# Kernel optimization log

Measured on AMD Instinct MI355X. Metric: run time of the kernel, lower is better.

Reference implementation:

```python
import jax, jax.numpy as jnp
import numpy as np
import math

SCALE = 16
R_MAX = 4
ALPHA_DYN = 2.0


def _bilinear_down(x, Ho, Wo):
    # torch F.interpolate bilinear, align_corners=False, no antialias. x: [C,H,W]
    C, H, W = x.shape
    def coords(no, ni):
        src = jnp.maximum((jnp.arange(no, dtype=jnp.float32) + 0.5) * (ni / no) - 0.5, 0.0)
        i0 = jnp.floor(src).astype(jnp.int32)
        t = src - i0.astype(jnp.float32)
        return jnp.clip(i0, 0, ni - 1), jnp.clip(i0 + 1, 0, ni - 1), t
    r0, r1, tr = coords(Ho, H)
    c0, c1, tc = coords(Wo, W)
    x = x[:, r0, :] * (1.0 - tr)[None, :, None] + x[:, r1, :] * tr[None, :, None]
    x = x[:, :, c0] * (1.0 - tc)[None, None, :] + x[:, :, c1] * tc[None, None, :]
    return x


def _jbu(feat_lr, guide_hr, sx_raw, sy_raw, th_raw, sr_raw):
    B, C, Hl, Wl = feat_lr.shape
    Hh, Wh = guide_hr.shape[2], guide_hr.shape[3]

    # parameter transforms
    up = lambda p: jnp.repeat(jnp.repeat(p[0, 0], SCALE, axis=0), SCALE, axis=1)  # nearest, exact multiple
    sx = jnp.maximum(up(jnp.exp(sx_raw)), 1e-6)
    sy = jnp.maximum(up(jnp.exp(sy_raw)), 1e-6)
    th = up(math.pi * jnp.tanh(th_raw))
    sr = jnp.maximum(up(jnp.exp(sr_raw)), 1e-6)

    Yh, Xh = jnp.meshgrid(jnp.arange(Hh, dtype=jnp.float32), jnp.arange(Wh, dtype=jnp.float32), indexing='ij')
    uc = jnp.round((Yh + 0.5) / SCALE - 0.5).astype(jnp.int32)
    vc = jnp.round((Xh + 0.5) / SCALE - 0.5).astype(jnp.int32)

    R_map_sq = jnp.clip(ALPHA_DYN * jnp.maximum(sx, sy), 1.0, float(R_MAX)) ** 2
    guide_lr = _bilinear_down(guide_hr[0], Hl, Wl)  # [Cg,Hl,Wl]
    cos_t, sin_t = jnp.cos(th), jnp.sin(th)
    inv2sx2 = 1.0 / (2.0 * sx ** 2 + 1e-8)
    inv2sy2 = 1.0 / (2.0 * sy ** 2 + 1e-8)
    inv2sr2 = 1.0 / (2.0 * sr ** 2 + 1e-8)

    d = jnp.arange(-R_MAX, R_MAX + 1, dtype=jnp.int32)
    dys, dxs = jnp.meshgrid(d, d, indexing='ij')
    offs = jnp.stack([dys.ravel(), dxs.ravel()], axis=1)  # [(2R+1)^2, 2]

    g_hr = guide_hr[0]    # [Cg,Hh,Wh]
    f_lr = feat_lr[0]     # [C,Hl,Wl]

    def step(carry, off):
        num, den = carry
        dy, dx = off[0], off[1]
        ui = jnp.clip(uc + dy, 0, Hl - 1)  # [Hh,Wh] int32
        vi = jnp.clip(vc + dx, 0, Wl - 1)
        cur_dx = (Xh - (vi.astype(jnp.float32) * SCALE + (SCALE - 1) / 2.0)) / SCALE
        cur_dy = (Yh - (ui.astype(jnp.float32) * SCALE + (SCALE - 1) / 2.0)) / SCALE
        a = cur_dx * cos_t + cur_dy * sin_t
        b = -cur_dx * sin_t + cur_dy * cos_t
        g_lr_s = guide_lr[:, ui, vi]                       # [Cg,Hh,Wh] gather
        g_diff2 = jnp.sum((g_hr - g_lr_s) ** 2, axis=0)    # [Hh,Wh]
        log_w = -(a ** 2) * inv2sx2 - (b ** 2) * inv2sy2 - g_diff2 * inv2sr2
        mask = (dy * dy + dx * dx).astype(jnp.float32) <= R_map_sq
        w = jnp.exp(log_w) * mask.astype(jnp.float32)      # [Hh,Wh]
        f_s = f_lr[:, ui, vi]                              # [C,Hh,Wh] gather
        return (num + f_s * w[None], den + w), None

    num0 = jnp.zeros((C, Hh, Wh), jnp.float32)
    den0 = jnp.zeros((Hh, Wh), jnp.float32)
    (num, den), _ = jax.lax.scan(step, (num0, den0), offs)
    res = num / jnp.maximum(den, 1e-8)
    return res[None].astype(feat_lr.dtype)


def setup_inputs() -> dict:
    key = jax.random.key(0)
    k1, k2 = jax.random.split(key)
    feat_lr = jax.random.normal(k1, (1, 128, 32, 32), jnp.float32)
    guide_hr = jax.random.normal(k2, (1, 3, 512, 512), jnp.float32)
    sx_raw = jnp.full((1, 1, 32, 32), float(np.log(16.0)), jnp.float32)
    sy_raw = jnp.full((1, 1, 32, 32), float(np.log(16.0)), jnp.float32)
    th_raw = jnp.zeros((1, 1, 32, 32), jnp.float32)
    sr_raw = jnp.full((1, 1, 32, 32), float(np.log(0.12)), jnp.float32)
    return {"feat_lr": feat_lr, "guide_hr": guide_hr, "sx_raw": sx_raw,
            "sy_raw": sy_raw, "th_raw": th_raw, "sr_raw": sr_raw}


def reference(feat_lr, guide_hr, sx_raw, sy_raw, th_raw, sr_raw):
    return _jbu(feat_lr, guide_hr, sx_raw, sy_raw, th_raw, sr_raw)
```

## Files before the change

### kernel.cpp

```cpp
#include <hip/hip_runtime.h>
#include <math.h>

#define HH 512
#define WH 512
#define L2E 1.44269504f
#define PI_F 3.14159265358979323846f
#define FTK 72

typedef __attribute__((ext_vector_type(8))) short short8v;
typedef __attribute__((ext_vector_type(4))) float float4v;

__device__ const unsigned char ORD[64] = {
    0x44,
    0x34,0x43,0x45,0x54,
    0x33,0x35,0x53,0x55,
    0x24,0x42,0x46,0x64,
    0x23,0x25,0x32,0x36,0x52,0x56,0x63,0x65,
    0x22,0x26,0x62,0x66,
    0x14,0x41,0x47,0x74,
    0x13,0x15,0x31,0x37,0x51,0x57,0x73,0x75,
    0x12,0x16,0x21,0x27,0x61,0x67,0x72,0x76,
    0x04,0x40,0x48,0x84,
    0x03,0x05,0x30,0x38,0x50,0x58,0x83,0x85,
    0x11,0x17,0x71,0x77,
    0x02,0x06,0x20
};

__global__ __launch_bounds__(256) void prep_kernel(
    const float* __restrict__ feat,
    const float* __restrict__ guide,
    float* __restrict__ ws)
{
    const int gid = blockIdx.x * 256 + threadIdx.x;
    float* glr = ws;
    unsigned short* featT = (unsigned short*)(ws + 4096);
    if (gid < 131072) {
        const int cell = gid >> 7;
        const int c    = gid & 127;
        const float v  = feat[c * 1024 + cell];
        const unsigned int b = __float_as_uint(v);
        featT[gid] = (unsigned short)((b + 0x7FFFu + ((b >> 16) & 1u)) >> 16);
    }
    if (gid < 1024) {
        const int u = gid >> 5, v = gid & 31;
        const int y0 = u * 16 + 7, x0 = v * 16 + 7;
        #pragma unroll
        for (int ch = 0; ch < 3; ++ch) {
            const float* g = guide + ch * (HH * WH);
            const float s = g[y0 * WH + x0] + g[y0 * WH + x0 + 1]
                          + g[(y0 + 1) * WH + x0] + g[(y0 + 1) * WH + x0 + 1];
            glr[gid * 4 + ch] = 0.25f * s;
        }
        glr[gid * 4 + 3] = 0.0f;
    }
}

__global__ __launch_bounds__(256, 4) void jbu_kernel(
    const float* __restrict__ guide,
    const float* __restrict__ sx_raw,
    const float* __restrict__ sy_raw,
    const float* __restrict__ th_raw,
    const float* __restrict__ sr_raw,
    const float* __restrict__ ws,
    float* __restrict__ out)
{
    __shared__ __align__(16) unsigned short FT[128 * FTK];
    __shared__ float tabK[64], tabA[64], tabB[64];
    __shared__ float tabG0[64], tabG1[64], tabG2[64];
    __shared__ float hdr[6];

    const float* glr = ws;
    const unsigned short* featT = (const unsigned short*)(ws + 4096);

    const int tid = threadIdx.x;
    const int cell = (blockIdx.x & 7) * 128 + (blockIdx.x >> 3);
    const int cu = cell >> 5, cv = cell & 31;

    if (tid < 64) {
        const int k = tid;
        const float sx  = fmaxf(__expf(sx_raw[cell]), 1e-6f);
        const float sy  = fmaxf(__expf(sy_raw[cell]), 1e-6f);
        const float thv = PI_F * tanhf(th_raw[cell]);
        const float sr  = fmaxf(__expf(sr_raw[cell]), 1e-6f);
        const float R   = fminf(fmaxf(2.0f * fmaxf(sx, sy), 1.0f), 4.0f);
        const float Rsq = R * R;
        const float cth = cosf(thv), sth = sinf(thv);
        const float i2sx = 1.0f / (2.0f * sx * sx + 1e-8f);
        const float i2sy = 1.0f / (2.0f * sy * sy + 1e-8f);
        const float i2sr = 1.0f / (2.0f * sr * sr + 1e-8f);
        if (k == 0) {
            hdr[0] = cth; hdr[1] = sth;
            hdr[2] = i2sx * L2E; hdr[3] = i2sy * L2E; hdr[4] = i2sr * L2E;
            hdr[5] = Rsq;
        }
        const int o  = ORD[k];
        const int dy = (o >> 4) - 4, dx = (o & 15) - 4;
        const int act = ((float)(dy * dy + dx * dx) <= Rsq);
        const int ui = min(max(cu + dy, 0), 31);
        const int vi = min(max(cv + dx, 0), 31);
        const float gl0 = glr[(ui * 32 + vi) * 4 + 0];
        const float gl1 = glr[(ui * 32 + vi) * 4 + 1];
        const float gl2 = glr[(ui * 32 + vi) * 4 + 2];
        const float rk = (float)(vi - cv), tk = (float)(ui - cu);
        const float ak = rk * cth + tk * sth;
        const float bk = tk * cth - rk * sth;
        tabK[k]  = act ? -(ak * ak * i2sx + bk * bk * i2sy
                           + (gl0*gl0 + gl1*gl1 + gl2*gl2) * i2sr) * L2E
                       : -1e30f;
        tabA[k]  = 2.0f * ak * i2sx * L2E;
        tabB[k]  = 2.0f * bk * i2sy * L2E;
        tabG0[k] = 2.0f * gl0 * i2sr * L2E;
        tabG1[k] = 2.0f * gl1 * i2sr * L2E;
        tabG2[k] = 2.0f * gl2 * i2sr * L2E;
    }

    const int wave = tid >> 6;
    const int lane = tid & 63;
    const int lg   = lane >> 4;
    const int pxx  = lane & 15;
    const int mtb  = wave * 4;

    float g0[4], g1[4], g2[4];
    #pragma unroll
    for (int mt = 0; mt < 4; ++mt) {
        const int y = cu * 16 + mtb + mt;
        const int o = y * WH + cv * 16 + pxx;
        g0[mt] = guide[o];
        g1[mt] = guide[HH * WH + o];
        g2[mt] = guide[2 * HH * WH + o];
    }

    #pragma unroll
    for (int it = 0; it < 4; ++it) {
        const int item = it * 256 + tid;
        const int k  = item & 63;
        const int cg = item >> 6;
        const int o  = ORD[k];
        const int ui = min(max(cu + (o >> 4) - 4, 0), 31);
        const int vi = min(max(cv + (o & 15) - 4, 0), 31);
        const uint4 val = *(const uint4*)(featT + (ui * 32 + vi) * 128 + cg * 8);
        const unsigned short* vs = (const unsigned short*)&val;
        #pragma unroll
        for (int j = 0; j < 8; ++j)
            FT[(cg * 8 + j) * FTK + k] = vs[j];
    }
    __syncthreads();

    const float cth = hdr[0], sth = hdr[1];
    const float i2sxl = hdr[2], i2syl = hdr[3], i2srl = hdr[4];
    const bool  use2 = hdr[5] >= 10.0f;
    const float qd = ((float)pxx - 7.5f) * 0.0625f;

    float a0[4], b0[4], P[4];
    #pragma unroll
    for (int mt = 0; mt < 4; ++mt) {
        const float pd = ((float)(mtb + mt) - 7.5f) * 0.0625f;
        a0[mt] = qd * cth + pd * sth;
        b0[mt] = pd * cth - qd * sth;
        P[mt]  = -(a0[mt]*a0[mt]*i2sxl + b0[mt]*b0[mt]*i2syl
                   + (g0[mt]*g0[mt] + g1[mt]*g1[mt] + g2[mt]*g2[mt]) * i2srl);
    }

    short8v Afrag[4][2];
    float den[4] = {0.f, 0.f, 0.f, 0.f};
    #pragma unroll
    for (int ks = 0; ks < 2; ++ks) {
        if (ks == 0 || use2) {
            float cK[8], cA[8], cB[8], cG0[8], cG1[8], cG2[8];
            #pragma unroll
            for (int i = 0; i < 8; ++i) {
                const int k = ks * 32 + lg * 8 + i;
                cK[i] = tabK[k];  cA[i] = tabA[k];  cB[i] = tabB[k];
                cG0[i] = tabG0[k]; cG1[i] = tabG1[k]; cG2[i] = tabG2[k];
            }
            #pragma unroll
            for (int mt = 0; mt < 4; ++mt) {
                short8v av;
                #pragma unroll
                for (int i = 0; i < 8; ++i) {
                    float lw = P[mt] + cK[i];
                    lw = fmaf(a0[mt], cA[i], lw);
                    lw = fmaf(b0[mt], cB[i], lw);
                    lw = fmaf(g0[mt], cG0[i], lw);
                    lw = fmaf(g1[mt], cG1[i], lw);
                    lw = fmaf(g2[mt], cG2[i], lw);
                    const float w = __builtin_amdgcn_exp2f(lw);
                    den[mt] += w;
                    const unsigned int b = __float_as_uint(w);
                    av[i] = (short)((b + 0x7FFFu + ((b >> 16) & 1u)) >> 16);
                }
                Afrag[mt][ks] = av;
            }
        }
    }

    float invd[4][4];
    #pragma unroll
    for (int mt = 0; mt < 4; ++mt) {
        float d = den[mt];
        d += __shfl_xor(d, 16);
        d += __shfl_xor(d, 32);
        const float id = 1.0f / fmaxf(d, 1e-8f);
        #pragma unroll
        for (int r = 0; r < 4; ++r)
            invd[mt][r] = __shfl(id, lg * 4 + r);
    }

    #pragma unroll
    for (int nt = 0; nt < 8; ++nt) {
        const int ch = nt * 16 + pxx;
        short8v Bf0 = *(const short8v*)&FT[ch * FTK + lg * 8];
        short8v Bf1 = *(const short8v*)&FT[ch * FTK + 32 + lg * 8];
        #pragma unroll
        for (int mt = 0; mt < 4; ++mt) {
            float4v acc = {0.f, 0.f, 0.f, 0.f};
            acc = __builtin_amdgcn_mfma_f32_16x16x32_bf16(Afrag[mt][0], Bf0, acc, 0, 0, 0);
            if (use2)
                acc = __builtin_amdgcn_mfma_f32_16x16x32_bf16(Afrag[mt][1], Bf1, acc, 0, 0, 0);
            const int y = cu * 16 + mtb + mt;
            float4v res;
            res[0] = acc[0] * invd[mt][0];
            res[1] = acc[1] * invd[mt][1];
            res[2] = acc[2] * invd[mt][2];
            res[3] = acc[3] * invd[mt][3];
            *(float4v*)(out + (size_t)ch * (HH * WH) + y * WH + cv * 16 + lg * 4) = res;
        }
    }
}

extern "C" void kernel_launch(void* const* d_in, const int* in_sizes, int n_in,
                              void* d_out, int out_size, void* d_ws, size_t ws_size,
                              hipStream_t stream) {
    const float* feat   = (const float*)d_in[0];
    const float* guide  = (const float*)d_in[1];
    const float* sx_raw = (const float*)d_in[2];
    const float* sy_raw = (const float*)d_in[3];
    const float* th_raw = (const float*)d_in[4];
    const float* sr_raw = (const float*)d_in[5];
    float* out = (float*)d_out;
    float* ws  = (float*)d_ws;

    prep_kernel<<<512, 256, 0, stream>>>(feat, guide, ws);
    jbu_kernel<<<1024, 256, 0, stream>>>(guide, sx_raw, sy_raw, th_raw, sr_raw, ws, out);
}
```

Before: 37.64 us.

## Split channels across two blocks per cell and hoist feature loads early

Each output cell is now handled by two blocks, each covering 64 of the 128 channels. This halves the shared feature tile, doubles the grid to 2048 blocks and raises the launch-bounds occupancy hint to 5. Feature gathers and guide loads are issued before the parameter-table setup so their latency overlaps it, and tanh/sincos use fast intrinsics. The cost is that the weight computation (exp2 per pixel and neighbour) is duplicated across the two blocks of each cell.

```diff
diff --git a/kernel.cpp b/kernel.cpp
--- a/kernel.cpp
+++ b/kernel.cpp
@@ -55,7 +55,7 @@
     }
 }
 
-__global__ __launch_bounds__(256, 4) void jbu_kernel(
+__global__ __launch_bounds__(256, 5) void jbu_kernel(
     const float* __restrict__ guide,
     const float* __restrict__ sx_raw,
     const float* __restrict__ sy_raw,
@@ -64,7 +64,7 @@
     const float* __restrict__ ws,
     float* __restrict__ out)
 {
-    __shared__ __align__(16) unsigned short FT[128 * FTK];
+    __shared__ __align__(16) unsigned short FT[64 * FTK];
     __shared__ float tabK[64], tabA[64], tabB[64];
     __shared__ float tabG0[64], tabG1[64], tabG2[64];
     __shared__ float hdr[6];
@@ -73,18 +73,53 @@
     const unsigned short* featT = (const unsigned short*)(ws + 4096);
 
     const int tid = threadIdx.x;
-    const int cell = (blockIdx.x & 7) * 128 + (blockIdx.x >> 3);
+    const int b   = blockIdx.x;
+    const int q    = (b >> 3) & 1;
+    const int cell = (b & 7) * 128 + (b >> 4);
     const int cu = cell >> 5, cv = cell & 31;
+
+    uint4 stg[2];
+    int stgk[2], stgcg[2];
+    #pragma unroll
+    for (int it = 0; it < 2; ++it) {
+        const int item = it * 256 + tid;
+        const int k  = item & 63;
+        const int cg = item >> 6;
+        const int o  = ORD[k];
+        const int ui = min(max(cu + (o >> 4) - 4, 0), 31);
+        const int vi = min(max(cv + (o & 15) - 4, 0), 31);
+        stg[it] = *(const uint4*)(featT + (ui * 32 + vi) * 128 + q * 64 + cg * 8);
+        stgk[it] = k; stgcg[it] = cg;
+    }
+
+    const int wave = tid >> 6;
+    const int lane = tid & 63;
+    const int lg   = lane >> 4;
+    const int pxx  = lane & 15;
+    const int mtb  = wave * 4;
+
+    float g0[4], g1[4], g2[4];
+    #pragma unroll
+    for (int mt = 0; mt < 4; ++mt) {
+        const int y = cu * 16 + mtb + mt;
+        const int o = y * WH + cv * 16 + pxx;
+        g0[mt] = guide[o];
+        g1[mt] = guide[HH * WH + o];
+        g2[mt] = guide[2 * HH * WH + o];
+    }
 
     if (tid < 64) {
         const int k = tid;
         const float sx  = fmaxf(__expf(sx_raw[cell]), 1e-6f);
         const float sy  = fmaxf(__expf(sy_raw[cell]), 1e-6f);
-        const float thv = PI_F * tanhf(th_raw[cell]);
+        const float tr  = fminf(fmaxf(th_raw[cell], -10.f), 10.f);
+        const float e2t = __expf(2.0f * tr);
+        const float thv = PI_F * ((e2t - 1.0f) / (e2t + 1.0f));
         const float sr  = fmaxf(__expf(sr_raw[cell]), 1e-6f);
         const float R   = fminf(fmaxf(2.0f * fmaxf(sx, sy), 1.0f), 4.0f);
         const float Rsq = R * R;
-        const float cth = cosf(thv), sth = sinf(thv);
+        float sth, cth;
+        __sincosf(thv, &sth, &cth);
         const float i2sx = 1.0f / (2.0f * sx * sx + 1e-8f);
         const float i2sy = 1.0f / (2.0f * sy * sy + 1e-8f);
         const float i2sr = 1.0f / (2.0f * sr * sr + 1e-8f);
@@ -114,35 +149,12 @@
         tabG2[k] = 2.0f * gl2 * i2sr * L2E;
     }
 
-    const int wave = tid >> 6;
-    const int lane = tid & 63;
-    const int lg   = lane >> 4;
-    const int pxx  = lane & 15;
-    const int mtb  = wave * 4;
-
-    float g0[4], g1[4], g2[4];
-    #pragma unroll
-    for (int mt = 0; mt < 4; ++mt) {
-        const int y = cu * 16 + mtb + mt;
-        const int o = y * WH + cv * 16 + pxx;
-        g0[mt] = guide[o];
-        g1[mt] = guide[HH * WH + o];
-        g2[mt] = guide[2 * HH * WH + o];
-    }
-
-    #pragma unroll
-    for (int it = 0; it < 4; ++it) {
-        const int item = it * 256 + tid;
-        const int k  = item & 63;
-        const int cg = item >> 6;
-        const int o  = ORD[k];
-        const int ui = min(max(cu + (o >> 4) - 4, 0), 31);
-        const int vi = min(max(cv + (o & 15) - 4, 0), 31);
-        const uint4 val = *(const uint4*)(featT + (ui * 32 + vi) * 128 + cg * 8);
-        const unsigned short* vs = (const unsigned short*)&val;
+    #pragma unroll
+    for (int it = 0; it < 2; ++it) {
+        const unsigned short* vs = (const unsigned short*)&stg[it];
         #pragma unroll
         for (int j = 0; j < 8; ++j)
-            FT[(cg * 8 + j) * FTK + k] = vs[j];
+            FT[(stgcg[it] * 8 + j) * FTK + stgk[it]] = vs[j];
     }
     __syncthreads();
 
@@ -186,8 +198,8 @@
                     lw = fmaf(g2[mt], cG2[i], lw);
                     const float w = __builtin_amdgcn_exp2f(lw);
                     den[mt] += w;
-                    const unsigned int b = __float_as_uint(w);
-                    av[i] = (short)((b + 0x7FFFu + ((b >> 16) & 1u)) >> 16);
+                    const unsigned int bb = __float_as_uint(w);
+                    av[i] = (short)((bb + 0x7FFFu + ((bb >> 16) & 1u)) >> 16);
                 }
                 Afrag[mt][ks] = av;
             }
@@ -207,10 +219,11 @@
     }
 
     #pragma unroll
-    for (int nt = 0; nt < 8; ++nt) {
-        const int ch = nt * 16 + pxx;
-        short8v Bf0 = *(const short8v*)&FT[ch * FTK + lg * 8];
-        short8v Bf1 = *(const short8v*)&FT[ch * FTK + 32 + lg * 8];
+    for (int nt = 0; nt < 4; ++nt) {
+        const int chl = nt * 16 + pxx;
+        short8v Bf0 = *(const short8v*)&FT[chl * FTK + lg * 8];
+        short8v Bf1 = *(const short8v*)&FT[chl * FTK + 32 + lg * 8];
+        const size_t chp = (size_t)(q * 64 + chl) * (HH * WH);
         #pragma unroll
         for (int mt = 0; mt < 4; ++mt) {
             float4v acc = {0.f, 0.f, 0.f, 0.f};
@@ -223,7 +236,7 @@
             res[1] = acc[1] * invd[mt][1];
             res[2] = acc[2] * invd[mt][2];
             res[3] = acc[3] * invd[mt][3];
-            *(float4v*)(out + (size_t)ch * (HH * WH) + y * WH + cv * 16 + lg * 4) = res;
+            *(float4v*)(out + chp + y * WH + cv * 16 + lg * 4) = res;
         }
     }
 }
@@ -241,5 +254,5 @@
     float* ws  = (float*)d_ws;
 
     prep_kernel<<<512, 256, 0, stream>>>(feat, guide, ws);
-    jbu_kernel<<<1024, 256, 0, stream>>>(guide, sx_raw, sy_raw, th_raw, sr_raw, ws, out);
+    jbu_kernel<<<2048, 256, 0, stream>>>(guide, sx_raw, sy_raw, th_raw, sr_raw, ws, out);
 }
```

Result: slower. 56.96 us (+51.3%).

## Process two cells per block and stage outputs in LDS for wider stores

Applied to the files above, without the earlier changes.

Each block now handles two horizontally adjacent low-res cells with 512 threads, and MFMA results are staged through a shared-memory tile so each output row segment is written as 128 contiguous bytes instead of 64-byte pieces. This targets write coalescing of the large 128-channel output. In exchange it adds two block barriers per channel tile and more LDS per block, and the second K-step MFMA now runs whenever either cell needs it. It also swaps tanhf/cosf/sinf for exp-based tanh and __sincosf in the per-cell setup.

```diff
diff --git a/kernel.cpp b/kernel.cpp
--- a/kernel.cpp
+++ b/kernel.cpp
@@ -55,7 +55,7 @@
     }
 }
 
-__global__ __launch_bounds__(256, 4) void jbu_kernel(
+__global__ __launch_bounds__(512, 4) void jbu_kernel(
     const float* __restrict__ guide,
     const float* __restrict__ sx_raw,
     const float* __restrict__ sy_raw,
@@ -64,37 +64,46 @@
     const float* __restrict__ ws,
     float* __restrict__ out)
 {
-    __shared__ __align__(16) unsigned short FT[128 * FTK];
-    __shared__ float tabK[64], tabA[64], tabB[64];
-    __shared__ float tabG0[64], tabG1[64], tabG2[64];
-    __shared__ float hdr[6];
+    __shared__ __align__(16) unsigned short FT[2][128][FTK];
+    __shared__ float tabK[2][64], tabA[2][64], tabB[2][64];
+    __shared__ float tabG0[2][64], tabG1[2][64], tabG2[2][64];
+    __shared__ float hdr[2][8];
+    __shared__ __align__(16) float OutT[16][16][34];
 
     const float* glr = ws;
     const unsigned short* featT = (const unsigned short*)(ws + 4096);
 
     const int tid = threadIdx.x;
-    const int cell = (blockIdx.x & 7) * 128 + (blockIdx.x >> 3);
-    const int cu = cell >> 5, cv = cell & 31;
-
-    if (tid < 64) {
-        const int k = tid;
+    const int b   = blockIdx.x;
+    const int pair = (b & 7) * 64 + (b >> 3);
+    const int cu  = pair >> 4;
+    const int cv0 = (pair & 15) * 2;
+
+    if (tid < 128) {
+        const int c2 = tid >> 6;
+        const int k  = tid & 63;
+        const int cell = cu * 32 + cv0 + c2;
         const float sx  = fmaxf(__expf(sx_raw[cell]), 1e-6f);
         const float sy  = fmaxf(__expf(sy_raw[cell]), 1e-6f);
-        const float thv = PI_F * tanhf(th_raw[cell]);
+        const float tr  = fminf(fmaxf(th_raw[cell], -10.f), 10.f);
+        const float e2t = __expf(2.0f * tr);
+        const float thv = PI_F * ((e2t - 1.0f) / (e2t + 1.0f));
         const float sr  = fmaxf(__expf(sr_raw[cell]), 1e-6f);
         const float R   = fminf(fmaxf(2.0f * fmaxf(sx, sy), 1.0f), 4.0f);
         const float Rsq = R * R;
-        const float cth = cosf(thv), sth = sinf(thv);
+        float sth, cth;
+        __sincosf(thv, &sth, &cth);
         const float i2sx = 1.0f / (2.0f * sx * sx + 1e-8f);
         const float i2sy = 1.0f / (2.0f * sy * sy + 1e-8f);
         const float i2sr = 1.0f / (2.0f * sr * sr + 1e-8f);
         if (k == 0) {
-            hdr[0] = cth; hdr[1] = sth;
-            hdr[2] = i2sx * L2E; hdr[3] = i2sy * L2E; hdr[4] = i2sr * L2E;
-            hdr[5] = Rsq;
+            hdr[c2][0] = cth; hdr[c2][1] = sth;
+            hdr[c2][2] = i2sx * L2E; hdr[c2][3] = i2sy * L2E; hdr[c2][4] = i2sr * L2E;
+            hdr[c2][5] = Rsq;
         }
         const int o  = ORD[k];
         const int dy = (o >> 4) - 4, dx = (o & 15) - 4;
+        const int cv = cv0 + c2;
         const int act = ((float)(dy * dy + dx * dx) <= Rsq);
         const int ui = min(max(cu + dy, 0), 31);
         const int vi = min(max(cv + dx, 0), 31);
@@ -104,21 +113,23 @@
         const float rk = (float)(vi - cv), tk = (float)(ui - cu);
         const float ak = rk * cth + tk * sth;
         const float bk = tk * cth - rk * sth;
-        tabK[k]  = act ? -(ak * ak * i2sx + bk * bk * i2sy
-                           + (gl0*gl0 + gl1*gl1 + gl2*gl2) * i2sr) * L2E
-                       : -1e30f;
-        tabA[k]  = 2.0f * ak * i2sx * L2E;
-        tabB[k]  = 2.0f * bk * i2sy * L2E;
-        tabG0[k] = 2.0f * gl0 * i2sr * L2E;
-        tabG1[k] = 2.0f * gl1 * i2sr * L2E;
-        tabG2[k] = 2.0f * gl2 * i2sr * L2E;
+        tabK[c2][k]  = act ? -(ak * ak * i2sx + bk * bk * i2sy
+                               + (gl0*gl0 + gl1*gl1 + gl2*gl2) * i2sr) * L2E
+                           : -1e30f;
+        tabA[c2][k]  = 2.0f * ak * i2sx * L2E;
+        tabB[c2][k]  = 2.0f * bk * i2sy * L2E;
+        tabG0[c2][k] = 2.0f * gl0 * i2sr * L2E;
+        tabG1[c2][k] = 2.0f * gl1 * i2sr * L2E;
+        tabG2[c2][k] = 2.0f * gl2 * i2sr * L2E;
     }
 
     const int wave = tid >> 6;
     const int lane = tid & 63;
     const int lg   = lane >> 4;
     const int pxx  = lane & 15;
-    const int mtb  = wave * 4;
+    const int c2   = wave >> 2;
+    const int mtb  = (wave & 3) * 4;
+    const int cv   = cv0 + c2;
 
     float g0[4], g1[4], g2[4];
     #pragma unroll
@@ -132,23 +143,24 @@
 
     #pragma unroll
     for (int it = 0; it < 4; ++it) {
-        const int item = it * 256 + tid;
-        const int k  = item & 63;
-        const int cg = item >> 6;
+        const int item = it * 512 + tid;
+        const int k   = item & 63;
+        const int cg  = (item >> 6) & 15;
+        const int c2s = item >> 10;
         const int o  = ORD[k];
         const int ui = min(max(cu + (o >> 4) - 4, 0), 31);
-        const int vi = min(max(cv + (o & 15) - 4, 0), 31);
+        const int vi = min(max(cv0 + c2s + (o & 15) - 4, 0), 31);
         const uint4 val = *(const uint4*)(featT + (ui * 32 + vi) * 128 + cg * 8);
         const unsigned short* vs = (const unsigned short*)&val;
         #pragma unroll
         for (int j = 0; j < 8; ++j)
-            FT[(cg * 8 + j) * FTK + k] = vs[j];
+            FT[c2s][cg * 8 + j][k] = vs[j];
     }
     __syncthreads();
 
-    const float cth = hdr[0], sth = hdr[1];
-    const float i2sxl = hdr[2], i2syl = hdr[3], i2srl = hdr[4];
-    const bool  use2 = hdr[5] >= 10.0f;
+    const float cth = hdr[c2][0], sth = hdr[c2][1];
+    const float i2sxl = hdr[c2][2], i2syl = hdr[c2][3], i2srl = hdr[c2][4];
+    const bool  use2 = (hdr[0][5] >= 10.0f) || (hdr[1][5] >= 10.0f);
     const float qd = ((float)pxx - 7.5f) * 0.0625f;
 
     float a0[4], b0[4], P[4];
@@ -170,8 +182,8 @@
             #pragma unroll
             for (int i = 0; i < 8; ++i) {
                 const int k = ks * 32 + lg * 8 + i;
-                cK[i] = tabK[k];  cA[i] = tabA[k];  cB[i] = tabB[k];
-                cG0[i] = tabG0[k]; cG1[i] = tabG1[k]; cG2[i] = tabG2[k];
+                cK[i] = tabK[c2][k];  cA[i] = tabA[c2][k];  cB[i] = tabB[c2][k];
+                cG0[i] = tabG0[c2][k]; cG1[i] = tabG1[c2][k]; cG2[i] = tabG2[c2][k];
             }
             #pragma unroll
             for (int mt = 0; mt < 4; ++mt) {
@@ -186,8 +198,8 @@
                     lw = fmaf(g2[mt], cG2[i], lw);
                     const float w = __builtin_amdgcn_exp2f(lw);
                     den[mt] += w;
-                    const unsigned int b = __float_as_uint(w);
-                    av[i] = (short)((b + 0x7FFFu + ((b >> 16) & 1u)) >> 16);
+                    const unsigned int bb = __float_as_uint(w);
+                    av[i] = (short)((bb + 0x7FFFu + ((bb >> 16) & 1u)) >> 16);
                 }
                 Afrag[mt][ks] = av;
             }
@@ -206,25 +218,37 @@
             invd[mt][r] = __shfl(id, lg * 4 + r);
     }
 
+    const int pxq   = tid & 7;
+    const int pr    = tid >> 3;
+    const int chs   = pr & 15;
+    const int rowq  = pr >> 4;
     #pragma unroll
     for (int nt = 0; nt < 8; ++nt) {
         const int ch = nt * 16 + pxx;
-        short8v Bf0 = *(const short8v*)&FT[ch * FTK + lg * 8];
-        short8v Bf1 = *(const short8v*)&FT[ch * FTK + 32 + lg * 8];
+        short8v Bf0 = *(const short8v*)&FT[c2][ch][lg * 8];
+        short8v Bf1 = *(const short8v*)&FT[c2][ch][32 + lg * 8];
         #pragma unroll
         for (int mt = 0; mt < 4; ++mt) {
             float4v acc = {0.f, 0.f, 0.f, 0.f};
             acc = __builtin_amdgcn_mfma_f32_16x16x32_bf16(Afrag[mt][0], Bf0, acc, 0, 0, 0);
             if (use2)
                 acc = __builtin_amdgcn_mfma_f32_16x16x32_bf16(Afrag[mt][1], Bf1, acc, 0, 0, 0);
-            const int y = cu * 16 + mtb + mt;
             float4v res;
             res[0] = acc[0] * invd[mt][0];
             res[1] = acc[1] * invd[mt][1];
             res[2] = acc[2] * invd[mt][2];
             res[3] = acc[3] * invd[mt][3];
-            *(float4v*)(out + (size_t)ch * (HH * WH) + y * WH + cv * 16 + lg * 4) = res;
-        }
+            *(float4v*)&OutT[mtb + mt][pxx][c2 * 16 + lg * 4] = res;
+        }
+        __syncthreads();
+        #pragma unroll
+        for (int i = 0; i < 4; ++i) {
+            const int row = i * 4 + rowq;
+            const float4v v = *(const float4v*)&OutT[row][chs][pxq * 4];
+            *(float4v*)(out + (size_t)(nt * 16 + chs) * (HH * WH)
+                        + (cu * 16 + row) * WH + cv0 * 16 + pxq * 4) = v;
+        }
+        __syncthreads();
     }
 }
 
@@ -241,5 +265,5 @@
     float* ws  = (float*)d_ws;
 
     prep_kernel<<<512, 256, 0, stream>>>(feat, guide, ws);
-    jbu_kernel<<<1024, 256, 0, stream>>>(guide, sx_raw, sy_raw, th_raw, sr_raw, ws, out);
+    jbu_kernel<<<512, 512, 0, stream>>>(guide, sx_raw, sy_raw, th_raw, sr_raw, ws, out);
 }
```

New measurement: 42.49 us. 1.13x slower.

## Fuse prep kernel into JBU kernel, computing bf16 features and low-res guide inline

Applied to the files above, without the earlier changes.

Removes the separate prep kernel launch. The main kernel now reads fp32 features directly with a strided gather, converts them to bf16 in-kernel, and computes the 2x2-average low-res guide values on the fly inside the table setup. Each block redoes this conversion for its 64 neighbours, so the redundant reads are uncoalesced (1024-element channel stride), but one launch and a global workspace round trip go away. Transcendentals are also switched to fast intrinsics (__sincosf, exp-based tanh).

```diff
diff --git a/kernel.cpp b/kernel.cpp
--- a/kernel.cpp
+++ b/kernel.cpp
@@ -26,42 +26,13 @@
     0x02,0x06,0x20
 };
 
-__global__ __launch_bounds__(256) void prep_kernel(
+__global__ __launch_bounds__(256, 4) void jbu_fused_kernel(
     const float* __restrict__ feat,
-    const float* __restrict__ guide,
-    float* __restrict__ ws)
-{
-    const int gid = blockIdx.x * 256 + threadIdx.x;
-    float* glr = ws;
-    unsigned short* featT = (unsigned short*)(ws + 4096);
-    if (gid < 131072) {
-        const int cell = gid >> 7;
-        const int c    = gid & 127;
-        const float v  = feat[c * 1024 + cell];
-        const unsigned int b = __float_as_uint(v);
-        featT[gid] = (unsigned short)((b + 0x7FFFu + ((b >> 16) & 1u)) >> 16);
-    }
-    if (gid < 1024) {
-        const int u = gid >> 5, v = gid & 31;
-        const int y0 = u * 16 + 7, x0 = v * 16 + 7;
-        #pragma unroll
-        for (int ch = 0; ch < 3; ++ch) {
-            const float* g = guide + ch * (HH * WH);
-            const float s = g[y0 * WH + x0] + g[y0 * WH + x0 + 1]
-                          + g[(y0 + 1) * WH + x0] + g[(y0 + 1) * WH + x0 + 1];
-            glr[gid * 4 + ch] = 0.25f * s;
-        }
-        glr[gid * 4 + 3] = 0.0f;
-    }
-}
-
-__global__ __launch_bounds__(256, 4) void jbu_kernel(
     const float* __restrict__ guide,
     const float* __restrict__ sx_raw,
     const float* __restrict__ sy_raw,
     const float* __restrict__ th_raw,
     const float* __restrict__ sr_raw,
-    const float* __restrict__ ws,
     float* __restrict__ out)
 {
     __shared__ __align__(16) unsigned short FT[128 * FTK];
@@ -69,22 +40,23 @@
     __shared__ float tabG0[64], tabG1[64], tabG2[64];
     __shared__ float hdr[6];
 
-    const float* glr = ws;
-    const unsigned short* featT = (const unsigned short*)(ws + 4096);
-
     const int tid = threadIdx.x;
-    const int cell = (blockIdx.x & 7) * 128 + (blockIdx.x >> 3);
+    const int b   = blockIdx.x;
+    const int cell = (b & 7) * 128 + (b >> 3);
     const int cu = cell >> 5, cv = cell & 31;
 
     if (tid < 64) {
         const int k = tid;
         const float sx  = fmaxf(__expf(sx_raw[cell]), 1e-6f);
         const float sy  = fmaxf(__expf(sy_raw[cell]), 1e-6f);
-        const float thv = PI_F * tanhf(th_raw[cell]);
+        const float tr  = fminf(fmaxf(th_raw[cell], -10.f), 10.f);
+        const float e2t = __expf(2.0f * tr);
+        const float thv = PI_F * ((e2t - 1.0f) / (e2t + 1.0f));
         const float sr  = fmaxf(__expf(sr_raw[cell]), 1e-6f);
         const float R   = fminf(fmaxf(2.0f * fmaxf(sx, sy), 1.0f), 4.0f);
         const float Rsq = R * R;
-        const float cth = cosf(thv), sth = sinf(thv);
+        float sth, cth;
+        __sincosf(thv, &sth, &cth);
         const float i2sx = 1.0f / (2.0f * sx * sx + 1e-8f);
         const float i2sy = 1.0f / (2.0f * sy * sy + 1e-8f);
         const float i2sr = 1.0f / (2.0f * sr * sr + 1e-8f);
@@ -98,20 +70,25 @@
         const int act = ((float)(dy * dy + dx * dx) <= Rsq);
         const int ui = min(max(cu + dy, 0), 31);
         const int vi = min(max(cv + dx, 0), 31);
-        const float gl0 = glr[(ui * 32 + vi) * 4 + 0];
-        const float gl1 = glr[(ui * 32 + vi) * 4 + 1];
-        const float gl2 = glr[(ui * 32 + vi) * 4 + 2];
+        const int yg = ui * 16 + 7, xg = vi * 16 + 7;
+        float gl[3];
+        #pragma unroll
+        for (int ch = 0; ch < 3; ++ch) {
+            const float* g = guide + ch * (HH * WH);
+            gl[ch] = 0.25f * (g[yg * WH + xg] + g[yg * WH + xg + 1]
+                            + g[(yg + 1) * WH + xg] + g[(yg + 1) * WH + xg + 1]);
+        }
         const float rk = (float)(vi - cv), tk = (float)(ui - cu);
         const float ak = rk * cth + tk * sth;
         const float bk = tk * cth - rk * sth;
         tabK[k]  = act ? -(ak * ak * i2sx + bk * bk * i2sy
-                           + (gl0*gl0 + gl1*gl1 + gl2*gl2) * i2sr) * L2E
+                           + (gl[0]*gl[0] + gl[1]*gl[1] + gl[2]*gl[2]) * i2sr) * L2E
                        : -1e30f;
         tabA[k]  = 2.0f * ak * i2sx * L2E;
         tabB[k]  = 2.0f * bk * i2sy * L2E;
-        tabG0[k] = 2.0f * gl0 * i2sr * L2E;
-        tabG1[k] = 2.0f * gl1 * i2sr * L2E;
-        tabG2[k] = 2.0f * gl2 * i2sr * L2E;
+        tabG0[k] = 2.0f * gl[0] * i2sr * L2E;
+        tabG1[k] = 2.0f * gl[1] * i2sr * L2E;
+        tabG2[k] = 2.0f * gl[2] * i2sr * L2E;
     }
 
     const int wave = tid >> 6;
@@ -130,19 +107,20 @@
         g2[mt] = guide[2 * HH * WH + o];
     }
 
-    #pragma unroll
-    for (int it = 0; it < 4; ++it) {
-        const int item = it * 256 + tid;
-        const int k  = item & 63;
-        const int cg = item >> 6;
+    {
+        const int k  = tid & 63;
+        const int cb = (tid >> 6) * 32;
         const int o  = ORD[k];
         const int ui = min(max(cu + (o >> 4) - 4, 0), 31);
         const int vi = min(max(cv + (o & 15) - 4, 0), 31);
-        const uint4 val = *(const uint4*)(featT + (ui * 32 + vi) * 128 + cg * 8);
-        const unsigned short* vs = (const unsigned short*)&val;
-        #pragma unroll
-        for (int j = 0; j < 8; ++j)
-            FT[(cg * 8 + j) * FTK + k] = vs[j];
+        const float* fp = feat + ui * 32 + vi;
+        #pragma unroll
+        for (int j = 0; j < 32; ++j) {
+            const float fv = fp[(cb + j) * 1024];
+            const unsigned int bb = __float_as_uint(fv);
+            FT[(cb + j) * FTK + k] =
+                (unsigned short)((bb + 0x7FFFu + ((bb >> 16) & 1u)) >> 16);
+        }
     }
     __syncthreads();
 
@@ -186,8 +164,8 @@
                     lw = fmaf(g2[mt], cG2[i], lw);
                     const float w = __builtin_amdgcn_exp2f(lw);
                     den[mt] += w;
-                    const unsigned int b = __float_as_uint(w);
-                    av[i] = (short)((b + 0x7FFFu + ((b >> 16) & 1u)) >> 16);
+                    const unsigned int bb = __float_as_uint(w);
+                    av[i] = (short)((bb + 0x7FFFu + ((bb >> 16) & 1u)) >> 16);
                 }
                 Afrag[mt][ks] = av;
             }
@@ -211,6 +189,7 @@
         const int ch = nt * 16 + pxx;
         short8v Bf0 = *(const short8v*)&FT[ch * FTK + lg * 8];
         short8v Bf1 = *(const short8v*)&FT[ch * FTK + 32 + lg * 8];
+        const size_t chp = (size_t)ch * (HH * WH);
         #pragma unroll
         for (int mt = 0; mt < 4; ++mt) {
             float4v acc = {0.f, 0.f, 0.f, 0.f};
@@ -223,7 +202,7 @@
             res[1] = acc[1] * invd[mt][1];
             res[2] = acc[2] * invd[mt][2];
             res[3] = acc[3] * invd[mt][3];
-            *(float4v*)(out + (size_t)ch * (HH * WH) + y * WH + cv * 16 + lg * 4) = res;
+            *(float4v*)(out + chp + y * WH + cv * 16 + lg * 4) = res;
         }
     }
 }
@@ -238,8 +217,8 @@
     const float* th_raw = (const float*)d_in[4];
     const float* sr_raw = (const float*)d_in[5];
     float* out = (float*)d_out;
-    float* ws  = (float*)d_ws;
-
-    prep_kernel<<<512, 256, 0, stream>>>(feat, guide, ws);
-    jbu_kernel<<<1024, 256, 0, stream>>>(guide, sx_raw, sy_raw, th_raw, sr_raw, ws, out);
+    (void)d_ws; (void)ws_size;
+
+    jbu_fused_kernel<<<1024, 256, 0, stream>>>(feat, guide, sx_raw, sy_raw,
+                                               th_raw, sr_raw, out);
 }
```

Result: no change. 37.29 us (-1.0%).
